# Optimization experiments

Hardware: AMD Instinct MI355X
Metric: run time of the kernel (lower is better)

Reference implementation:

```python
import jax, jax.numpy as jnp
import numpy as np
from jax import lax

B, C_IN, T = 64, 40, 8192

def conv1d(x, w, b):
    # x: [B,C,T], w: [O,I,K] (torch Conv1d layout), stride 2, VALID padding
    y = lax.conv_general_dilated(x, w, window_strides=(2,), padding='VALID',
                                 dimension_numbers=('NCH', 'OIH', 'NCH'))
    return y + b[None, :, None]

def avgpool2(x):
    # AvgPool1d(kernel=2, stride=2): pairwise mean, drop trailing odd element
    t2 = x.shape[-1] // 2
    return x[..., :2 * t2].reshape(x.shape[0], x.shape[1], t2, 2).mean(-1)

def setup_inputs():
    key = jax.random.key(0)
    ks = jax.random.split(key, 24)
    def w_init(k, shape, fan_in):
        return jax.random.normal(k, shape, jnp.float32) * (1.0 / np.sqrt(fan_in))
    inp = {}
    inp['x_input'] = jax.random.normal(ks[0], (B, C_IN, T), jnp.float32)
    # per-sample valid lengths in [2048, 8192] so the deep strided stack leaves >=1 frame
    inp['len_mask'] = 2048 + jax.random.randint(ks[1], (B,), 0, T - 2048 + 1, dtype=jnp.int32)
    convs = [(96, C_IN, 10), (96, 96, 5), (96, 96, 5), (96, 96, 5), (96, 96, 5), (96, 96, 5), (128, 96, 3)]
    for i, (o, ci, k) in enumerate(convs):
        inp[f'w{i+1}'] = w_init(ks[2 + 2 * i], (o, ci, k), ci * k)
        inp[f'b{i+1}'] = jnp.zeros((o,), jnp.float32)
    lins = [(128, 128), (64, 128), (5, 64)]
    for i, (o, ci) in enumerate(lins):
        inp[f'lw{i+1}'] = w_init(ks[16 + 2 * i], (o, ci), ci)
        inp[f'lb{i+1}'] = jnp.zeros((o,), jnp.float32)
    return inp

def reference(x_input, len_mask, w1, b1, w2, b2, w3, b3, w4, b4, w5, b5, w6, b6, w7, b7,
              lw1, lb1, lw2, lb2, lw3, lb3):
    # Batched masked equivalent of the per-sample ragged loop: for VALID stride-2 convs,
    # output position j depends only on inputs < valid length when j < valid out-length,
    # so we run batched convs on padded input and track per-sample valid lengths.
    Lv = len_mask.astype(jnp.int32)
    x = jax.nn.relu(conv1d(x_input, w1, b1)); Lv = (Lv - 10) // 2 + 1
    x = jax.nn.relu(conv1d(x, w2, b2));       Lv = (Lv - 5) // 2 + 1
    x = jax.nn.relu(conv1d(x, w3, b3));       Lv = (Lv - 5) // 2 + 1
    # cnn_1d_top (dropout in eval mode = identity)
    x = conv1d(x, w4, b4);        Lv = (Lv - 5) // 2 + 1
    x = jax.nn.relu(avgpool2(x)); Lv = Lv // 2
    x = conv1d(x, w5, b5);        Lv = (Lv - 5) // 2 + 1
    x = jax.nn.relu(avgpool2(x)); Lv = Lv // 2
    x = jax.nn.relu(conv1d(x, w6, b6)); Lv = (Lv - 5) // 2 + 1
    x = jax.nn.relu(conv1d(x, w7, b7)); Lv = (Lv - 3) // 2 + 1
    # AdaptiveMaxPool1d(1) over each sample's valid region
    mask = jnp.arange(x.shape[-1])[None, :] < Lv[:, None]          # [B, T_out]
    x = jnp.max(jnp.where(mask[:, None, :], x, -jnp.inf), axis=-1)  # [B, 128]
    # out1_top MLP head
    h = jax.nn.relu(x @ lw1.T + lb1)
    h = jax.nn.relu(h @ lw2.T + lb2)
    return h @ lw3.T + lb3
```

## Files before the change

### kernel.cpp

```cpp
#include <hip/hip_runtime.h>
#include <hip/hip_bf16.h>
#include <math.h>


typedef __attribute__((ext_vector_type(8))) _Float16 f16x8;
typedef __attribute__((ext_vector_type(4))) float f32x4;

__device__ __forceinline__ unsigned short f2h_bits(float f) {
    union { _Float16 h; unsigned short u; } cv;
    cv.h = (_Float16)f;
    return cv.u;
}

template<int KEFF, int CI, int NBLK, bool IN_FP32, bool RELU, bool OUT_F16,
         bool POOL, int PIPE>
__global__ __launch_bounds__(512, 2)
void conv_nb(const unsigned short* __restrict__ xh,
             const unsigned short* __restrict__ wpk,
             const float* __restrict__ bias,
             unsigned short* __restrict__ yh,
             float* __restrict__ yf,
             int Tin, int Tout)
{
    constexpr int CO    = 96;
    constexpr int NTHR  = 512;
    constexpr int GTOT  = CI * KEFF;
    constexpr int STEPS = (GTOT + 31) / 32;
    constexpr int RD    = NBLK + KEFF / 2;
    constexpr int NTW   = NBLK / 64;
    constexpr int TOT   = CI * RD;
    constexpr int NIT   = (TOT + NTHR - 1) / NTHR;
    constexpr int PH    = (32 % KEFF == 0) ? 1 : (((32 * 3) % KEFF == 0) ? 3 : 5);
    constexpr int PERRD = (32 * PH / KEFF) * RD;

    __shared__ unsigned int Bs[TOT];

    const int tid  = threadIdx.x;
    const int lane = tid & 63;
    const int wave = tid >> 6;
    const int mg   = wave & 1;
    const int tg   = wave >> 1;
    const int quad = lane >> 4;
    const int l16  = lane & 15;
    const int wc0  = tg * (NBLK / 4);

    const int nT = (Tout + NBLK - 1) / NBLK;
    const int b  = blockIdx.x / nT;
    const int t0 = (blockIdx.x % nT) * NBLK;

    const float* xf = (const float*)xh;
    const unsigned int* xb = (const unsigned int*)xh + (((size_t)b * CI * Tin) >> 1);
    const int rowd = Tin >> 1;

    #pragma unroll
    for (int it = 0; it < NIT; ++it) {
        int i = tid + it * NTHR;
        if (i < TOT) {
            int r = (unsigned)i / (unsigned)RD, d = i - r * RD;
            unsigned int v;
            if (IN_FP32) {
                int e = 2 * (t0 + d);
                if (e > Tin - 2) e = Tin - 2;
                const float* src = xf + ((size_t)b * CI + r) * Tin + e;
                float2 w = *(const float2*)src;
                v = (unsigned int)f2h_bits(w.x) | ((unsigned int)f2h_bits(w.y) << 16);
            } else {
                int dd = t0 + d;
                if (dd > rowd - 1) dd = rowd - 1;
                v = *(xb + (size_t)r * rowd + dd);
            }
            Bs[i] = v;
        }
    }
    __syncthreads();

    int offb[PH][4];
    #pragma unroll
    for (int ph = 0; ph < PH; ++ph)
        #pragma unroll
        for (int p = 0; p < 4; ++p) {
            int g = 32 * ph + quad * 8 + 2 * p;
            unsigned ci = (unsigned)g / (unsigned)KEFF;
            unsigned dwo = ((unsigned)g - ci * (unsigned)KEFF) >> 1;
            offb[ph][p] = (int)ci * RD + wc0 + l16 + (int)dwo;
        }

    f32x4 acc[3][NTW];
    #pragma unroll
    for (int mt = 0; mt < 3; ++mt)
        #pragma unroll
        for (int nt = 0; nt < NTW; ++nt) acc[mt][nt] = (f32x4)0.f;

    union BvU { unsigned int u[4]; f16x8 v; };

    auto load_step = [&](int s, BvU (&Bv)[NTW], f16x8 (&Ah)[3], f16x8 (&Al)[3]) {
        if (32 * (s + 1) <= GTOT) {
            #pragma unroll
            for (int nt = 0; nt < NTW; ++nt)
                #pragma unroll
                for (int p = 0; p < 4; ++p)
                    Bv[nt].u[p] = Bs[offb[s % PH][p] + (s / PH) * PERRD + nt * 16];
        } else {
            #pragma unroll
            for (int nt = 0; nt < NTW; ++nt)
                #pragma unroll
                for (int p = 0; p < 4; ++p) {
                    int g = 32 * s + quad * 8 + 2 * p;
                    if (g > GTOT - 2) g = GTOT - 2;
                    unsigned ci = (unsigned)g / (unsigned)KEFF;
                    unsigned dwo = ((unsigned)g - ci * (unsigned)KEFF) >> 1;
                    Bv[nt].u[p] = Bs[(int)ci * RD + wc0 + l16 + (int)dwo + nt * 16];
                }
        }
        const unsigned short* ap = wpk + (size_t)s * 6144 + (size_t)(mg * 3) * 512
                                 + (size_t)lane * 8;
        #pragma unroll
        for (int mt = 0; mt < 3; ++mt) {
            Ah[mt] = *(const f16x8*)(ap + mt * 512);
            Al[mt] = *(const f16x8*)(ap + 3072 + mt * 512);
        }
    };
    auto mfma_step = [&](BvU (&Bv)[NTW], f16x8 (&Ah)[3], f16x8 (&Al)[3]) {
        #pragma unroll
        for (int mt = 0; mt < 3; ++mt)
            #pragma unroll
            for (int nt = 0; nt < NTW; ++nt)
                acc[mt][nt] = __builtin_amdgcn_mfma_f32_16x16x32_f16(Ah[mt], Bv[nt].v, acc[mt][nt], 0, 0, 0);
        #pragma unroll
        for (int mt = 0; mt < 3; ++mt)
            #pragma unroll
            for (int nt = 0; nt < NTW; ++nt)
                acc[mt][nt] = __builtin_amdgcn_mfma_f32_16x16x32_f16(Al[mt], Bv[nt].v, acc[mt][nt], 0, 0, 0);
    };

    if (PIPE == 0) {
        #pragma unroll
        for (int s = 0; s < STEPS; ++s) {
            BvU Bv[NTW];
            f16x8 Ah[3], Al[3];
            load_step(s, Bv, Ah, Al);
            mfma_step(Bv, Ah, Al);
        }
    } else {
        BvU  Bv0[NTW], Bv1[NTW];
        f16x8 Ah0[3], Al0[3], Ah1[3], Al1[3];

        load_step(0, Bv0, Ah0, Al0);
        #pragma unroll
        for (int s = 0; s < STEPS; ++s) {
            if (s + 1 < STEPS) {
                if (((s + 1) & 1) == 0) load_step(s + 1, Bv0, Ah0, Al0);
                else                    load_step(s + 1, Bv1, Ah1, Al1);
            }
            __builtin_amdgcn_sched_barrier(0);
            __builtin_amdgcn_s_setprio(1);
            if ((s & 1) == 0) mfma_step(Bv0, Ah0, Al0);
            else              mfma_step(Bv1, Ah1, Al1);
            __builtin_amdgcn_s_setprio(0);
            __builtin_amdgcn_sched_barrier(0);
        }
    }

    #pragma unroll
    for (int mt = 0; mt < 3; ++mt) {
        #pragma unroll
        for (int r = 0; r < 4; ++r) {
            int o = (mg * 3 + mt) * 16 + quad * 4 + r;
            float bv = bias[o];
            #pragma unroll
            for (int nt = 0; nt < NTW; ++nt) {
                int t = t0 + wc0 + nt * 16 + l16;
                float v = acc[mt][nt][r] + bv;
                if (RELU) v = fmaxf(v, 0.f);
                if (POOL) {
                    float sum = v + __shfl_xor(v, 1, 64);
                    if ((lane & 1) == 0 && t + 1 < Tout) {
                        float pr = fmaxf(0.5f * sum, 0.f);
                        size_t pidx = ((size_t)b * CO + o) * (Tout >> 1) + (t >> 1);
                        if (OUT_F16) yh[pidx] = f2h_bits(pr);
                        else         yf[pidx] = pr;
                    }
                } else if (OUT_F16) {
                    unsigned int h = f2h_bits(v);
                    unsigned int hp = (unsigned int)__shfl_xor((int)h, 1, 64);
                    if ((lane & 1) == 0 && t + 1 < Tout) {
                        size_t base = ((size_t)b * CO + o) * Tout + t;
                        *(unsigned int*)(yh + base) = h | (hp << 16);
                    }
                } else if (t < Tout) {
                    yf[((size_t)b * CO + o) * Tout + t] = v;
                }
            }
        }
    }
}

__device__ __forceinline__ void repack_img(const float* __restrict__ w,
                                           unsigned short* __restrict__ wpk,
                                           int idx, int KP, int KW, int CI)
{
    int j = idx & 7, lane = (idx >> 3) & 63, g = idx >> 9;
    int c = g / 24, r = g % 24;
    int mt = r % 6, sh = r / 6;
    int half = sh & 1, s = sh >> 1;
    int S  = c * 2 + s;
    int kg = S * 32 + (lane >> 4) * 8 + j;
    int o  = mt * 16 + (lane & 15);
    int ci = kg / KP, k = kg - ci * KP;
    float val = (ci < CI && k < KW) ? w[((size_t)o * CI + ci) * KW + k] : 0.f;
    _Float16 hh = (_Float16)val;
    union { _Float16 h; unsigned short u; } cv;
    cv.h = (half == 0) ? hh : (_Float16)(val - (float)hh);
    wpk[idx] = cv.u;
}
__device__ __forceinline__ void repack_okc(const float* __restrict__ w,
                                           float* __restrict__ wr,
                                           int idx, int CI, int K, int CO)
{
    int o = idx % CO; int rem = idx / CO; int k = rem % K; int ci = rem / K;
    wr[idx] = w[((size_t)o * CI + ci) * K + k];
}

__global__ void repack_all(const float* w1, const float* w2, const float* w3,
                           const float* w4, const float* w5, const float* w6,
                           const float* w7,
                           unsigned short* p1, unsigned short* p2,
                           unsigned short* p3, unsigned short* p4,
                           unsigned short* p5, float* r6, float* r7)
{
    int idx = blockIdx.x * 256 + threadIdx.x;
    if (idx < 79872)  { repack_img(w1, p1, idx, 10, 10, 40); return; }
    idx -= 79872;
    if (idx < 110592) { repack_img(w2, p2, idx, 6, 5, 96); return; }
    idx -= 110592;
    if (idx < 110592) { repack_img(w3, p3, idx, 6, 5, 96); return; }
    idx -= 110592;
    if (idx < 110592) { repack_img(w4, p4, idx, 6, 5, 96); return; }
    idx -= 110592;
    if (idx < 110592) { repack_img(w5, p5, idx, 6, 5, 96); return; }
    idx -= 110592;
    if (idx < 46080)  { repack_okc(w6, r6, idx, 96, 5, 96); return; }
    idx -= 46080;
    if (idx < 36864)  { repack_okc(w7, r7, idx, 96, 3, 128); return; }
}

__global__ __launch_bounds__(256)
void conv6_k(const float* __restrict__ y5p, const float* __restrict__ w6r,
             const float* __restrict__ b6, float* __restrict__ y6)
{
    __shared__ float s5[96 * 62];
    const int b = blockIdx.x >> 2, ob = blockIdx.x & 3;
    const int tid = threadIdx.x;
    for (int i = tid; i < 96 * 62; i += 256) s5[i] = y5p[(size_t)b * 96 * 62 + i];
    __syncthreads();

    const int wave = __builtin_amdgcn_readfirstlane(tid >> 6);
    const int t = tid & 63;
    if (t < 29) {
        const int o0 = ob * 24 + wave * 6;
        float a[6];
        #pragma unroll
        for (int oo = 0; oo < 6; oo++) a[oo] = 0.f;
        for (int ci = 0; ci < 96; ci++) {
            float xr[5];
            #pragma unroll
            for (int k = 0; k < 5; k++) xr[k] = s5[ci * 62 + 2 * t + k];
            #pragma unroll
            for (int k = 0; k < 5; k++) {
                const float* wp = w6r + (ci * 5 + k) * 96 + o0;
                #pragma unroll
                for (int oo = 0; oo < 6; oo++)
                    a[oo] = fmaf(wp[oo], xr[k], a[oo]);
            }
        }
        #pragma unroll
        for (int oo = 0; oo < 6; oo++)
            y6[((size_t)b * 96 + o0 + oo) * 29 + t] = fmaxf(a[oo] + b6[o0 + oo], 0.f);
    }
}

__global__ __launch_bounds__(256)
void tail2(const float* __restrict__ y6,
           const float* __restrict__ w7r, const float* __restrict__ b7,
           const int* __restrict__ lens,
           const float* __restrict__ lw1, const float* __restrict__ lb1,
           const float* __restrict__ lw2, const float* __restrict__ lb2,
           const float* __restrict__ lw3, const float* __restrict__ lb3,
           float* __restrict__ out)
{
    __shared__ float s6[96 * 29 + 8];
    __shared__ float s7[128 * 14];
    __shared__ float feat[128], h1[128], h2[64];

    const int b = blockIdx.x, tid = threadIdx.x;
    for (int i = tid; i < 96 * 29; i += 256) s6[i] = y6[(size_t)b * 96 * 29 + i];
    __syncthreads();

    const int wave = __builtin_amdgcn_readfirstlane(tid >> 6);
    const int lane = tid & 63;
    const int sub  = lane >> 4;
    const int tl   = lane & 15;
    {
        float a[32];
        #pragma unroll
        for (int oo = 0; oo < 32; oo++) a[oo] = 0.f;
        const int ci0 = sub * 24;
        for (int ci = ci0; ci < ci0 + 24; ci++) {
            float xr[3];
            #pragma unroll
            for (int k = 0; k < 3; k++) xr[k] = s6[ci * 29 + 2 * tl + k];
            #pragma unroll
            for (int k = 0; k < 3; k++) {
                const float* wp = w7r + (ci * 3 + k) * 128 + wave * 32;
                #pragma unroll
                for (int oo = 0; oo < 32; oo++)
                    a[oo] = fmaf(wp[oo], xr[k], a[oo]);
            }
        }
        #pragma unroll
        for (int oo = 0; oo < 32; oo++) {
            float v = a[oo];
            v += __shfl_xor(v, 16, 64);
            v += __shfl_xor(v, 32, 64);
            if (sub == 0 && tl < 14) {
                int o = wave * 32 + oo;
                s7[o * 14 + tl] = fmaxf(v + b7[o], 0.f);
            }
        }
    }
    __syncthreads();

    if (tid < 128) {
        int L = lens[b];
        L = (L - 10) / 2 + 1;
        L = (L - 5) / 2 + 1;
        L = (L - 5) / 2 + 1;
        L = (L - 5) / 2 + 1;
        L = L / 2;
        L = (L - 5) / 2 + 1;
        L = L / 2;
        L = (L - 5) / 2 + 1;
        L = (L - 3) / 2 + 1;
        float m = -INFINITY;
        for (int t = 0; t < L; t++) m = fmaxf(m, s7[tid * 14 + t]);
        feat[tid] = m;
    }
    __syncthreads();

    if (tid < 128) {
        float s = lb1[tid];
        for (int i = 0; i < 128; i++) s = fmaf(lw1[tid * 128 + i], feat[i], s);
        h1[tid] = fmaxf(s, 0.f);
    }
    __syncthreads();
    if (tid < 64) {
        float s = lb2[tid];
        for (int i = 0; i < 128; i++) s = fmaf(lw2[tid * 128 + i], h1[i], s);
        h2[tid] = fmaxf(s, 0.f);
    }
    __syncthreads();
    if (tid < 5) {
        float s = lb3[tid];
        for (int i = 0; i < 64; i++) s = fmaf(lw3[tid * 64 + i], h2[i], s);
        out[b * 5 + tid] = s;
    }
}

extern "C" void kernel_launch(void* const* d_in, const int* in_sizes, int n_in,
                              void* d_out, int out_size, void* d_ws, size_t ws_size,
                              hipStream_t stream)
{
    const float* x    = (const float*)d_in[0];
    const int*   lens = (const int*)  d_in[1];
    const float* w1 = (const float*)d_in[2];   const float* b1 = (const float*)d_in[3];
    const float* w2 = (const float*)d_in[4];   const float* b2 = (const float*)d_in[5];
    const float* w3 = (const float*)d_in[6];   const float* b3 = (const float*)d_in[7];
    const float* w4 = (const float*)d_in[8];   const float* b4 = (const float*)d_in[9];
    const float* w5 = (const float*)d_in[10];  const float* b5 = (const float*)d_in[11];
    const float* w6 = (const float*)d_in[12];  const float* b6 = (const float*)d_in[13];
    const float* w7 = (const float*)d_in[14];  const float* b7 = (const float*)d_in[15];
    const float* lw1 = (const float*)d_in[16]; const float* lb1 = (const float*)d_in[17];
    const float* lw2 = (const float*)d_in[18]; const float* lb2 = (const float*)d_in[19];
    const float* lw3 = (const float*)d_in[20]; const float* lb3 = (const float*)d_in[21];
    float* out = (float*)d_out;
    char*  W   = (char*)d_ws;

    size_t off = 0;
    auto take = [&](size_t bytes) {
        size_t o = off; off = (off + bytes + 255) & ~(size_t)255; return o;
    };
    size_t o_y3h = take(((size_t)64 * 96 * 1020 + 2048) * 2);
    size_t o_y4h = take(((size_t)64 * 96 * 254 + 2048) * 2);
    size_t o_y5p = take((size_t)64 * 96 * 62 * 4 + 1024);
    size_t o_y6  = take((size_t)64 * 96 * 29 * 4);
    size_t o_wp1 = take((size_t)79872 * 2);
    size_t o_wp2 = take((size_t)110592 * 2);
    size_t o_wp3 = take((size_t)110592 * 2);
    size_t o_wp4 = take((size_t)110592 * 2);
    size_t o_wp5 = take((size_t)110592 * 2);
    size_t o_w6r = take((size_t)46080 * 4);
    size_t o_w7r = take((size_t)36864 * 4);
    size_t persist = off;

    auto chunk_bytes = [&](int Bc) -> size_t {
        size_t s = 0;
        s += ((size_t)Bc * 96 * 4092 + 2048) * 2 + 256;
        s += ((size_t)Bc * 96 * 2044 + 2048) * 2 + 256;
        return s;
    };
    int Bc = 64;
    while (Bc > 1 && persist + chunk_bytes(Bc) > ws_size) Bc >>= 1;
    size_t o_y1h = take(((size_t)Bc * 96 * 4092 + 2048) * 2);
    size_t o_y2h = take(((size_t)Bc * 96 * 2044 + 2048) * 2);

    auto US = [&](size_t o) { return (unsigned short*)(W + o); };
    auto FP = [&](size_t o) { return (float*)(W + o); };

    repack_all<<<dim3((605184 + 255) / 256), 256, 0, stream>>>(
        w1, w2, w3, w4, w5, w6, w7,
        US(o_wp1), US(o_wp2), US(o_wp3), US(o_wp4), US(o_wp5),
        FP(o_w6r), FP(o_w7r));

    const int nchunks = 64 / Bc;
    for (int c = 0; c < nchunks; c++) {
        const float* xc = x + (size_t)c * Bc * 40 * 8192;

        conv_nb<10, 40, 256, true, true, true, false, 0><<<dim3(Bc * 16), 512, 0, stream>>>(
            (const unsigned short*)xc, US(o_wp1), b1, US(o_y1h), nullptr, 8192, 4092);
        conv_nb< 6, 96, 128, false, true, true, false, 1><<<dim3(Bc * 16), 512, 0, stream>>>(
            US(o_y1h), US(o_wp2), b2, US(o_y2h), nullptr, 4092, 2044);
        unsigned short* y3h_c = US(o_y3h) + (size_t)c * Bc * 96 * 1020;
        conv_nb< 6, 96, 128, false, true, true, false, 1><<<dim3(Bc * 8), 512, 0, stream>>>(
            US(o_y2h), US(o_wp3), b3, y3h_c, nullptr, 2044, 1020);
    }

    conv_nb<6, 96, 64, false, false, true, true, 1><<<dim3(64 * 8), 512, 0, stream>>>(
        US(o_y3h), US(o_wp4), b4, US(o_y4h), nullptr, 1020, 508);

    conv_nb<6, 96, 64, false, false, false, true, 1><<<dim3(64 * 2), 512, 0, stream>>>(
        US(o_y4h), US(o_wp5), b5, nullptr, FP(o_y5p), 254, 125);

    conv6_k<<<dim3(256), 256, 0, stream>>>(FP(o_y5p), FP(o_w6r), b6, FP(o_y6));

    tail2<<<dim3(64), 256, 0, stream>>>(
        FP(o_y6), FP(o_w7r), b7, lens, lw1, lb1, lw2, lb2, lw3, lb3, out);
}
```

Baseline: 378.7 us.

## Stage conv2 input in channel-split phases and widen its time tile

Adds a PHASES template parameter that stages the input tile into shared memory in chunks of input channels, with a sync between phases, so a wider tile fits in the same shared memory. Conv2 switches to a 256-wide time tile with two phases and half as many blocks, and drops its software pipelining (PIPE=0). The goal is more weight reuse per staged tile and fewer blocks, at the cost of an extra barrier, more accumulators per thread, and losing load/MFMA overlap in conv2.

```diff
diff --git a/kernel.cpp b/kernel.cpp
--- a/kernel.cpp
+++ b/kernel.cpp
@@ -13,7 +13,7 @@
 }
 
 template<int KEFF, int CI, int NBLK, bool IN_FP32, bool RELU, bool OUT_F16,
-         bool POOL, int PIPE>
+         bool POOL, int PIPE, int PHASES>
 __global__ __launch_bounds__(512, 2)
 void conv_nb(const unsigned short* __restrict__ xh,
              const unsigned short* __restrict__ wpk,
@@ -26,14 +26,16 @@
     constexpr int NTHR  = 512;
     constexpr int GTOT  = CI * KEFF;
     constexpr int STEPS = (GTOT + 31) / 32;
+    constexpr int SH    = STEPS / PHASES;
+    constexpr int CIH   = CI / PHASES;
     constexpr int RD    = NBLK + KEFF / 2;
     constexpr int NTW   = NBLK / 64;
-    constexpr int TOT   = CI * RD;
-    constexpr int NIT   = (TOT + NTHR - 1) / NTHR;
+    constexpr int TOTH  = CIH * RD;
+    constexpr int NIT   = (TOTH + NTHR - 1) / NTHR;
     constexpr int PH    = (32 % KEFF == 0) ? 1 : (((32 * 3) % KEFF == 0) ? 3 : 5);
     constexpr int PERRD = (32 * PH / KEFF) * RD;
 
-    __shared__ unsigned int Bs[TOT];
+    __shared__ unsigned int Bs[TOTH];
 
     const int tid  = threadIdx.x;
     const int lane = tid & 63;
@@ -52,27 +54,29 @@
     const unsigned int* xb = (const unsigned int*)xh + (((size_t)b * CI * Tin) >> 1);
     const int rowd = Tin >> 1;
 
-    #pragma unroll
-    for (int it = 0; it < NIT; ++it) {
-        int i = tid + it * NTHR;
-        if (i < TOT) {
-            int r = (unsigned)i / (unsigned)RD, d = i - r * RD;
-            unsigned int v;
-            if (IN_FP32) {
-                int e = 2 * (t0 + d);
-                if (e > Tin - 2) e = Tin - 2;
-                const float* src = xf + ((size_t)b * CI + r) * Tin + e;
-                float2 w = *(const float2*)src;
-                v = (unsigned int)f2h_bits(w.x) | ((unsigned int)f2h_bits(w.y) << 16);
-            } else {
-                int dd = t0 + d;
-                if (dd > rowd - 1) dd = rowd - 1;
-                v = *(xb + (size_t)r * rowd + dd);
-            }
-            Bs[i] = v;
-        }
-    }
-    __syncthreads();
+    auto stageB = [&](int ph) {
+        const int ci0 = ph * CIH;
+        #pragma unroll
+        for (int it = 0; it < NIT; ++it) {
+            int i = tid + it * NTHR;
+            if (i < TOTH) {
+                int r = (unsigned)i / (unsigned)RD, d = i - r * RD;
+                unsigned int v;
+                if (IN_FP32) {
+                    int e = 2 * (t0 + d);
+                    if (e > Tin - 2) e = Tin - 2;
+                    const float* src = xf + ((size_t)b * CI + ci0 + r) * Tin + e;
+                    float2 w = *(const float2*)src;
+                    v = (unsigned int)f2h_bits(w.x) | ((unsigned int)f2h_bits(w.y) << 16);
+                } else {
+                    int dd = t0 + d;
+                    if (dd > rowd - 1) dd = rowd - 1;
+                    v = *(xb + (size_t)(ci0 + r) * rowd + dd);
+                }
+                Bs[i] = v;
+            }
+        }
+    };
 
     int offb[PH][4];
     #pragma unroll
@@ -93,26 +97,26 @@
 
     union BvU { unsigned int u[4]; f16x8 v; };
 
-    auto load_step = [&](int s, BvU (&Bv)[NTW], f16x8 (&Ah)[3], f16x8 (&Al)[3]) {
-        if (32 * (s + 1) <= GTOT) {
+    auto load_step = [&](int sg, int sl, BvU (&Bv)[NTW], f16x8 (&Ah)[3], f16x8 (&Al)[3]) {
+        if (32 * (sg + 1) <= GTOT) {
             #pragma unroll
             for (int nt = 0; nt < NTW; ++nt)
                 #pragma unroll
                 for (int p = 0; p < 4; ++p)
-                    Bv[nt].u[p] = Bs[offb[s % PH][p] + (s / PH) * PERRD + nt * 16];
+                    Bv[nt].u[p] = Bs[offb[sl % PH][p] + (sl / PH) * PERRD + nt * 16];
         } else {
             #pragma unroll
             for (int nt = 0; nt < NTW; ++nt)
                 #pragma unroll
                 for (int p = 0; p < 4; ++p) {
-                    int g = 32 * s + quad * 8 + 2 * p;
+                    int g = 32 * sg + quad * 8 + 2 * p;
                     if (g > GTOT - 2) g = GTOT - 2;
                     unsigned ci = (unsigned)g / (unsigned)KEFF;
                     unsigned dwo = ((unsigned)g - ci * (unsigned)KEFF) >> 1;
                     Bv[nt].u[p] = Bs[(int)ci * RD + wc0 + l16 + (int)dwo + nt * 16];
                 }
         }
-        const unsigned short* ap = wpk + (size_t)s * 6144 + (size_t)(mg * 3) * 512
+        const unsigned short* ap = wpk + (size_t)sg * 6144 + (size_t)(mg * 3) * 512
                                  + (size_t)lane * 8;
         #pragma unroll
         for (int mt = 0; mt < 3; ++mt) {
@@ -133,31 +137,38 @@
                 acc[mt][nt] = __builtin_amdgcn_mfma_f32_16x16x32_f16(Al[mt], Bv[nt].v, acc[mt][nt], 0, 0, 0);
     };
 
-    if (PIPE == 0) {
-        #pragma unroll
-        for (int s = 0; s < STEPS; ++s) {
-            BvU Bv[NTW];
-            f16x8 Ah[3], Al[3];
-            load_step(s, Bv, Ah, Al);
-            mfma_step(Bv, Ah, Al);
-        }
-    } else {
-        BvU  Bv0[NTW], Bv1[NTW];
-        f16x8 Ah0[3], Al0[3], Ah1[3], Al1[3];
-
-        load_step(0, Bv0, Ah0, Al0);
-        #pragma unroll
-        for (int s = 0; s < STEPS; ++s) {
-            if (s + 1 < STEPS) {
-                if (((s + 1) & 1) == 0) load_step(s + 1, Bv0, Ah0, Al0);
-                else                    load_step(s + 1, Bv1, Ah1, Al1);
-            }
-            __builtin_amdgcn_sched_barrier(0);
-            __builtin_amdgcn_s_setprio(1);
-            if ((s & 1) == 0) mfma_step(Bv0, Ah0, Al0);
-            else              mfma_step(Bv1, Ah1, Al1);
-            __builtin_amdgcn_s_setprio(0);
-            __builtin_amdgcn_sched_barrier(0);
+    #pragma unroll
+    for (int ph2 = 0; ph2 < PHASES; ++ph2) {
+        if (ph2 > 0) __syncthreads();
+        stageB(ph2);
+        __syncthreads();
+
+        if (PIPE == 0) {
+            #pragma unroll
+            for (int s2 = 0; s2 < SH; ++s2) {
+                BvU Bv[NTW];
+                f16x8 Ah[3], Al[3];
+                load_step(ph2 * SH + s2, s2, Bv, Ah, Al);
+                mfma_step(Bv, Ah, Al);
+            }
+        } else {
+            BvU  Bv0[NTW], Bv1[NTW];
+            f16x8 Ah0[3], Al0[3], Ah1[3], Al1[3];
+
+            load_step(ph2 * SH, 0, Bv0, Ah0, Al0);
+            #pragma unroll
+            for (int s2 = 0; s2 < SH; ++s2) {
+                if (s2 + 1 < SH) {
+                    if (((s2 + 1) & 1) == 0) load_step(ph2 * SH + s2 + 1, s2 + 1, Bv0, Ah0, Al0);
+                    else                     load_step(ph2 * SH + s2 + 1, s2 + 1, Bv1, Ah1, Al1);
+                }
+                __builtin_amdgcn_sched_barrier(0);
+                __builtin_amdgcn_s_setprio(1);
+                if ((s2 & 1) == 0) mfma_step(Bv0, Ah0, Al0);
+                else               mfma_step(Bv1, Ah1, Al1);
+                __builtin_amdgcn_s_setprio(0);
+                __builtin_amdgcn_sched_barrier(0);
+            }
         }
     }
 
@@ -425,19 +436,19 @@
     for (int c = 0; c < nchunks; c++) {
         const float* xc = x + (size_t)c * Bc * 40 * 8192;
 
-        conv_nb<10, 40, 256, true, true, true, false, 0><<<dim3(Bc * 16), 512, 0, stream>>>(
+        conv_nb<10, 40, 256, true, true, true, false, 0, 1><<<dim3(Bc * 16), 512, 0, stream>>>(
             (const unsigned short*)xc, US(o_wp1), b1, US(o_y1h), nullptr, 8192, 4092);
-        conv_nb< 6, 96, 128, false, true, true, false, 1><<<dim3(Bc * 16), 512, 0, stream>>>(
+        conv_nb< 6, 96, 256, false, true, true, false, 0, 2><<<dim3(Bc * 8), 512, 0, stream>>>(
             US(o_y1h), US(o_wp2), b2, US(o_y2h), nullptr, 4092, 2044);
         unsigned short* y3h_c = US(o_y3h) + (size_t)c * Bc * 96 * 1020;
-        conv_nb< 6, 96, 128, false, true, true, false, 1><<<dim3(Bc * 8), 512, 0, stream>>>(
+        conv_nb< 6, 96, 128, false, true, true, false, 1, 1><<<dim3(Bc * 8), 512, 0, stream>>>(
             US(o_y2h), US(o_wp3), b3, y3h_c, nullptr, 2044, 1020);
     }
 
-    conv_nb<6, 96, 64, false, false, true, true, 1><<<dim3(64 * 8), 512, 0, stream>>>(
+    conv_nb<6, 96, 64, false, false, true, true, 1, 1><<<dim3(64 * 8), 512, 0, stream>>>(
         US(o_y3h), US(o_wp4), b4, US(o_y4h), nullptr, 1020, 508);
 
-    conv_nb<6, 96, 64, false, false, false, true, 1><<<dim3(64 * 2), 512, 0, stream>>>(
+    conv_nb<6, 96, 64, false, false, false, true, 1, 1><<<dim3(64 * 2), 512, 0, stream>>>(
         US(o_y4h), US(o_wp5), b5, nullptr, FP(o_y5p), 254, 125);
 
     conv6_k<<<dim3(256), 256, 0, stream>>>(FP(o_y5p), FP(o_w6r), b6, FP(o_y6));
```

Result: no change. 384.0 us (+1.4%).
